# Kernel tuning notes

Measured on AMD Instinct MI355X. Metric: run time of the kernel, lower is better.

## Reference

```python
import jax, jax.numpy as jnp
import numpy as np

B, T, C, L = 256, 512, 256, 64
NEG = -1e30  # log-space 'zero'
BLANK = 0


def setup_inputs() -> dict:
    key = jax.random.key(0)
    k1, k2, k3, k4 = jax.random.split(key, 4)
    logits = jax.random.normal(k1, (B, T, C), dtype=jnp.float32)
    targets = jax.random.randint(k2, (B, L), 1, C)            # labels never equal blank (0)
    input_lengths = jax.random.randint(k3, (B,), T - 100, T + 1)
    target_lengths = jax.random.randint(k4, (B,), L // 2, L + 1)
    return dict(logits=logits, targets=targets,
                input_lengths=input_lengths, target_lengths=target_lengths)


def _ctc_loss(logits, targets, input_lengths, target_lengths):
    Bb, Tt, Cc = logits.shape
    Ll = targets.shape[1]
    S = 2 * Ll + 1  # extended label length (blanks interleaved)

    # fused log_softmax over vocab (original does permute then log_softmax; same math)
    logp = jax.nn.log_softmax(logits, axis=-1)  # [B,T,C]

    # extended target sequence: blank, y1, blank, y2, ..., blank
    ext = jnp.zeros((Bb, S), jnp.int32).at[:, 1::2].set(targets.astype(jnp.int32))
    # gather log-probs of extended labels for every timestep: [B,T,S]
    lp_ext = jnp.take_along_axis(logp, jnp.broadcast_to(ext[:, None, :], (Bb, Tt, S)), axis=2)

    # skip transition s-2 -> s allowed iff ext[s] != blank and ext[s] != ext[s-2]
    skip = jnp.zeros((Bb, S), bool).at[:, 2:].set(
        (ext[:, 2:] != BLANK) & (ext[:, 2:] != ext[:, :-2]))

    # alpha at t=0
    alpha0 = (jnp.full((Bb, S), NEG, dtype=logits.dtype)
              .at[:, 0].set(lp_ext[:, 0, 0])
              .at[:, 1].set(lp_ext[:, 0, 1]))

    neg1 = jnp.full((Bb, 1), NEG, dtype=logits.dtype)
    neg2 = jnp.full((Bb, 2), NEG, dtype=logits.dtype)

    def step(alpha, inputs):
        lp_t, t = inputs  # lp_t: [B,S]
        a1 = alpha
        a2 = jnp.concatenate([neg1, alpha[:, :-1]], axis=1)
        a3 = jnp.where(skip, jnp.concatenate([neg2, alpha[:, :-2]], axis=1), NEG)
        new = jnp.logaddexp(jnp.logaddexp(a1, a2), a3) + lp_t
        new = jnp.maximum(new, NEG)  # keep impossible paths bounded
        # freeze alpha for batch rows whose input sequence already ended
        alpha = jnp.where((t < input_lengths)[:, None], new, alpha)
        return alpha, None

    ts = jnp.arange(1, Tt)
    alphaT, _ = jax.lax.scan(step, alpha0, (jnp.swapaxes(lp_ext, 0, 1)[1:], ts))

    tl = target_lengths.astype(jnp.int32)
    a_last = jnp.take_along_axis(alphaT, (2 * tl)[:, None], axis=1)[:, 0]
    a_prev = jnp.take_along_axis(alphaT, (2 * tl - 1)[:, None], axis=1)[:, 0]
    loss = -jnp.logaddexp(a_last, a_prev)            # [B]
    loss = jnp.where(loss > 1e20, 0.0, loss)          # zero_infinity=True
    # reduction='mean': per-sample loss divided by target length, then batch mean
    return (loss / tl.astype(loss.dtype)).mean()


def reference(logits, targets, input_lengths, target_lengths):
    return _ctc_loss(logits, targets, input_lengths, target_lengths)
```

## Files before the change

### kernel.cpp

```cpp
#include <hip/hip_runtime.h>

#define B_ 256
#define T_ 512
#define C_ 256
#define L_ 64
#define S_ 129
#define TCH 64
#define LOG2E 1.44269504f
#define LN2 0.69314718f

template <int CTRL>
__device__ __forceinline__ int dpp_mov_i32(int x) {
    return __builtin_amdgcn_update_dpp(0, x, CTRL, 0xF, 0xF, true);
}

__device__ __forceinline__ double shr1d(double x) {
    int2 u = __builtin_bit_cast(int2, x);
    u.x = dpp_mov_i32<0x138>(u.x);
    u.y = dpp_mov_i32<0x138>(u.y);
    return __builtin_bit_cast(double, u);
}

template <int CTRL>
__device__ __forceinline__ double dpp_mov_f64(double x) {
    int2 u = __builtin_bit_cast(int2, x);
    u.x = dpp_mov_i32<CTRL>(u.x);
    u.y = dpp_mov_i32<CTRL>(u.y);
    return __builtin_bit_cast(double, u);
}

__device__ __forceinline__ float wave_sum(float x) {
#define DPPADD(ctrl)                                                          \
    x += __builtin_bit_cast(float, dpp_mov_i32<ctrl>(__builtin_bit_cast(int, x)));
    DPPADD(0x111) DPPADD(0x112) DPPADD(0x114)
    DPPADD(0x118) DPPADD(0x142) DPPADD(0x143)
#undef DPPADD
    return __builtin_bit_cast(float,
        __builtin_amdgcn_readlane(__builtin_bit_cast(int, x), 63));
}

__device__ __forceinline__ double wave_max_d(double x) {
    x = fmax(x, dpp_mov_f64<0x111>(x));
    x = fmax(x, dpp_mov_f64<0x112>(x));
    x = fmax(x, dpp_mov_f64<0x114>(x));
    x = fmax(x, dpp_mov_f64<0x118>(x));
    x = fmax(x, dpp_mov_f64<0x142>(x));
    x = fmax(x, dpp_mov_f64<0x143>(x));
    int2 u = __builtin_bit_cast(int2, x);
    u.x = __builtin_amdgcn_readlane(u.x, 63);
    u.y = __builtin_amdgcn_readlane(u.y, 63);
    return __builtin_bit_cast(double, u);
}

__device__ __forceinline__ void rescale(double& a0, double& a1, double& a2, int& e) {
    const double m = wave_max_d(fmax(fmax(a0, a1), a2));
    const int hi = __builtin_bit_cast(int2, m).y;
    int ex = ((hi >> 20) & 0x7ff) - 1023;
    if (m == 0.0) ex = 0;
    e += ex;
    int2 fb; fb.x = 0; fb.y = (1023 - ex) << 20;
    const double f = __builtin_bit_cast(double, fb);
    a0 *= f; a1 *= f; a2 *= f;
}

__device__ __forceinline__ float log2_pos(double a) {
    if (a == 0.0) return -1e30f;
    int2 u = __builtin_bit_cast(int2, a);
    const int ex = ((u.y >> 20) & 0x7ff) - 1023;
    u.y = (u.y & 0x800FFFFF) | (1023 << 20);
    const float mf = (float)__builtin_bit_cast(double, u);
    return __log2f(mf) + (float)ex;
}

__global__ __launch_bounds__(576) void k_fused(const float* __restrict__ logits,
                                               const int* __restrict__ targets,
                                               const int* __restrict__ in_len,
                                               const int* __restrict__ tg_len,
                                               float* __restrict__ out) {
    const int b = blockIdx.x;
    const int w = threadIdx.x >> 6;
    const int l = threadIdx.x & 63;

    __shared__ float Pb[2][TCH][64];
    __shared__ float Po[2][TCH][64];
    __shared__ int   tgt_sh[L_];
    __shared__ float alpha_sh[S_];

    if (threadIdx.x < L_) tgt_sh[threadIdx.x] = targets[(b << 6) + threadIdx.x];
    __syncthreads();

    const int len = in_len[b];
    double a0 = 0.0, a1 = 0.0, a2 = 0.0;
    int scale_total = 0;
    bool skip = false;
    if (w == 0) {
        const int tc = tgt_sh[l];
        const int tp = __shfl_up(tc, 1);
        skip = (l >= 1) && (tc != tp);
        __builtin_amdgcn_s_setprio(1);
    }
    const int mytgt = tgt_sh[l];

    const size_t rowbase = (size_t)b * T_;

    for (int k = 0; k < 9; ++k) {
        if (w > 0 && k < 8) {
            const int tt0 = (w - 1) * 8;
            float4 v[8];
            float  lv[8];
            #pragma unroll
            for (int r = 0; r < 8; ++r) {
                const int t = k * TCH + tt0 + r;
                v[r]  = ((const float4*)logits)[(rowbase + t) * 64 + l];
                lv[r] = logits[(rowbase + t) * C_ + mytgt];
            }
            #pragma unroll
            for (int r = 0; r < 8; ++r) {
                const int tt = tt0 + r;
                const float e0 = exp2f(v[r].x * LOG2E);
                const float e1 = exp2f(v[r].y * LOG2E);
                const float e2 = exp2f(v[r].z * LOG2E);
                const float e3 = exp2f(v[r].w * LOG2E);
                const float stot = wave_sum(e0 + e1 + e2 + e3);
                const float rs = __builtin_amdgcn_rcpf(stot);
                const float eb = __builtin_bit_cast(float,
                    __builtin_amdgcn_readfirstlane(__builtin_bit_cast(int, e0)));
                Pb[k & 1][tt][l] = eb * rs;
                Po[k & 1][tt][l] = exp2f(lv[r] * LOG2E) * rs;
            }
        }
        if (w == 0 && k >= 1) {
            const int kb = (k - 1) & 1;
            const int base = (k - 1) * TCH;
            float pba[8], poa[8], pbb[8], pob[8];
            #pragma unroll
            for (int j = 0; j < 8; ++j) { pba[j] = Pb[kb][j][l]; poa[j] = Po[kb][j][l]; }
            if (base == 0) {
                a0 = (l == 0) ? (double)pba[0] : 0.0;
                a1 = (l == 0) ? (double)poa[0] : 0.0;
                a2 = 0.0;
            }
            for (int g = 0; g < 8; ++g) {
                if (g < 7) {
                    #pragma unroll
                    for (int j = 0; j < 8; ++j) {
                        pbb[j] = Pb[kb][(g + 1) * 8 + j][l];
                        pob[j] = Po[kb][(g + 1) * 8 + j][l];
                    }
                }
                #pragma unroll
                for (int j = 0; j < 8; ++j) {
                    const int t = base + g * 8 + j;
                    if (t >= 1 && t < len) {
                        const double p = shr1d(a1);
                        const double c = skip ? p : 0.0;
                        const double a0n = (a0 + p) * (double)pba[j];
                        const double a1n = ((a1 + a0) + c) * (double)poa[j];
                        const double a2n = (a2 + a1) * (double)pba[j];
                        a0 = a0n; a1 = a1n; a2 = a2n;
                    }
                }
                if (g == 3 || g == 7) rescale(a0, a1, a2, scale_total);
                if (g < 7) {
                    #pragma unroll
                    for (int j = 0; j < 8; ++j) { pba[j] = pbb[j]; poa[j] = pob[j]; }
                }
            }
        }
        __syncthreads();
    }

    if (w == 0) {
        alpha_sh[2 * l]     = log2_pos(a0);
        alpha_sh[2 * l + 1] = log2_pos(a1);
        if (l == 63) alpha_sh[128] = log2_pos(a2);
    }
    __syncthreads();
    if (threadIdx.x == 0) {
        const int tl = tg_len[b];
        const float al = alpha_sh[2 * tl];
        const float ap = alpha_sh[2 * tl - 1];
        const float m  = fmaxf(al, ap);
        const float lse2 = m + __log2f(exp2f(al - m) + exp2f(ap - m));
        float loss = -LN2 * (lse2 + (float)scale_total);
        if (!(loss < 1e20f)) loss = 0.0f;
        atomicAdd(out, loss / (float)tl * (1.0f / (float)B_));
    }
}

extern "C" void kernel_launch(void* const* d_in, const int* in_sizes, int n_in,
                              void* d_out, int out_size, void* d_ws, size_t ws_size,
                              hipStream_t stream) {
    const float* logits  = (const float*)d_in[0];
    const int*   targets = (const int*)d_in[1];
    const int*   in_len  = (const int*)d_in[2];
    const int*   tg_len  = (const int*)d_in[3];
    float*       out     = (float*)d_out;

    (void)hipMemsetAsync(d_out, 0, sizeof(float), stream);
    k_fused<<<B_, 576, 0, stream>>>(logits, targets, in_len, tg_len, out);
}
```

Measured before the change: 204.2 us.

## Prefetch next logits chunk, gather target probs via LDS, pack P as float2

The producer waves now prefetch the next chunk's logits rows into registers while computing the current chunk. The separate scattered global load of the target-label logit is replaced by reading the already-computed exponentials from a small LDS staging buffer. The blank and label probabilities are packed into one float2 LDS array, so the recurrence wave issues fewer LDS loads. The cost is more registers per producer thread, extra LDS writes and reads per timestep, and a possible race on the reused rb4 slots, since a wave may read another lane's freshly written values without a barrier.

```diff
diff --git a/kernel.cpp b/kernel.cpp
--- a/kernel.cpp
+++ b/kernel.cpp
@@ -81,8 +81,8 @@
     const int w = threadIdx.x >> 6;
     const int l = threadIdx.x & 63;
 
-    __shared__ float Pb[2][TCH][64];
-    __shared__ float Po[2][TCH][64];
+    __shared__ float2 P[2][TCH][64];
+    __shared__ float4 rb4[8][2][64];
     __shared__ int   tgt_sh[L_];
     __shared__ float alpha_sh[S_];
 
@@ -103,50 +103,60 @@
 
     const size_t rowbase = (size_t)b * T_;
 
+    float4 va[8];
+    if (w > 0) {
+        const int tt0 = (w - 1) * 8;
+        #pragma unroll
+        for (int r = 0; r < 8; ++r)
+            va[r] = ((const float4*)logits)[(rowbase + tt0 + r) * 64 + l];
+    }
+
     for (int k = 0; k < 9; ++k) {
         if (w > 0 && k < 8) {
             const int tt0 = (w - 1) * 8;
-            float4 v[8];
-            float  lv[8];
-            #pragma unroll
-            for (int r = 0; r < 8; ++r) {
-                const int t = k * TCH + tt0 + r;
-                v[r]  = ((const float4*)logits)[(rowbase + t) * 64 + l];
-                lv[r] = logits[(rowbase + t) * C_ + mytgt];
+            float4 vb[8];
+            if (k < 7) {
+                #pragma unroll
+                for (int r = 0; r < 8; ++r) {
+                    const int t = (k + 1) * TCH + tt0 + r;
+                    vb[r] = ((const float4*)logits)[(rowbase + t) * 64 + l];
+                }
             }
             #pragma unroll
             for (int r = 0; r < 8; ++r) {
                 const int tt = tt0 + r;
-                const float e0 = exp2f(v[r].x * LOG2E);
-                const float e1 = exp2f(v[r].y * LOG2E);
-                const float e2 = exp2f(v[r].z * LOG2E);
-                const float e3 = exp2f(v[r].w * LOG2E);
-                const float stot = wave_sum(e0 + e1 + e2 + e3);
+                float4 e;
+                e.x = exp2f(va[r].x * LOG2E);
+                e.y = exp2f(va[r].y * LOG2E);
+                e.z = exp2f(va[r].z * LOG2E);
+                e.w = exp2f(va[r].w * LOG2E);
+                rb4[w - 1][r & 1][l] = e;
+                const float stot = wave_sum(e.x + e.y + e.z + e.w);
                 const float rs = __builtin_amdgcn_rcpf(stot);
                 const float eb = __builtin_bit_cast(float,
-                    __builtin_amdgcn_readfirstlane(__builtin_bit_cast(int, e0)));
-                Pb[k & 1][tt][l] = eb * rs;
-                Po[k & 1][tt][l] = exp2f(lv[r] * LOG2E) * rs;
-            }
+                    __builtin_amdgcn_readfirstlane(__builtin_bit_cast(int, e.x)));
+                const float eo = ((const float*)&rb4[w - 1][r & 1][0])[mytgt];
+                float2 pq; pq.x = eb * rs; pq.y = eo * rs;
+                P[k & 1][tt][l] = pq;
+            }
+            #pragma unroll
+            for (int r = 0; r < 8; ++r) va[r] = vb[r];
         }
         if (w == 0 && k >= 1) {
             const int kb = (k - 1) & 1;
             const int base = (k - 1) * TCH;
-            float pba[8], poa[8], pbb[8], pob[8];
+            float2 pa[8], pn[8];
             #pragma unroll
-            for (int j = 0; j < 8; ++j) { pba[j] = Pb[kb][j][l]; poa[j] = Po[kb][j][l]; }
+            for (int j = 0; j < 8; ++j) pa[j] = P[kb][j][l];
             if (base == 0) {
-                a0 = (l == 0) ? (double)pba[0] : 0.0;
-                a1 = (l == 0) ? (double)poa[0] : 0.0;
+                a0 = (l == 0) ? (double)pa[0].x : 0.0;
+                a1 = (l == 0) ? (double)pa[0].y : 0.0;
                 a2 = 0.0;
             }
             for (int g = 0; g < 8; ++g) {
                 if (g < 7) {
                     #pragma unroll
-                    for (int j = 0; j < 8; ++j) {
-                        pbb[j] = Pb[kb][(g + 1) * 8 + j][l];
-                        pob[j] = Po[kb][(g + 1) * 8 + j][l];
-                    }
+                    for (int j = 0; j < 8; ++j) pn[j] = P[kb][(g + 1) * 8 + j][l];
                 }
                 #pragma unroll
                 for (int j = 0; j < 8; ++j) {
@@ -154,16 +164,16 @@
                     if (t >= 1 && t < len) {
                         const double p = shr1d(a1);
                         const double c = skip ? p : 0.0;
-                        const double a0n = (a0 + p) * (double)pba[j];
-                        const double a1n = ((a1 + a0) + c) * (double)poa[j];
-                        const double a2n = (a2 + a1) * (double)pba[j];
+                        const double a0n = (a0 + p) * (double)pa[j].x;
+                        const double a1n = ((a1 + a0) + c) * (double)pa[j].y;
+                        const double a2n = (a2 + a1) * (double)pa[j].x;
                         a0 = a0n; a1 = a1n; a2 = a2n;
                     }
                 }
                 if (g == 3 || g == 7) rescale(a0, a1, a2, scale_total);
                 if (g < 7) {
                     #pragma unroll
-                    for (int j = 0; j < 8; ++j) { pba[j] = pbb[j]; poa[j] = pob[j]; }
+                    for (int j = 0; j < 8; ++j) pa[j] = pn[j];
                 }
             }
         }
```

New measurement: 203.5 us. About the same (-0.3%).

## Split fused CTC kernel into softmax-gather pass and fp16-fed alpha recursion

Applied to the files above, without the earlier changes.

Replaces the single producer/consumer kernel with two launches. The first is a fully parallel softmax kernel that writes scaled blank and label probabilities as packed fp16 into workspace. The second is a single-wave-per-batch alpha recursion that register-prefetches 32 timesteps ahead from global memory and rescales once per chunk. The aim is to remove the in-block synchronisation, shared-memory staging and serialisation of softmax behind the recurrence. In exchange it adds a global round trip, fp16 precision loss mitigated by a power-of-two prescale that is corrected in the loss, and a dependence on the workspace buffer.

```diff
diff --git a/kernel.cpp b/kernel.cpp
--- a/kernel.cpp
+++ b/kernel.cpp
@@ -5,9 +5,19 @@
 #define C_ 256
 #define L_ 64
 #define S_ 129
-#define TCH 64
+#define CH 32
 #define LOG2E 1.44269504f
 #define LN2 0.69314718f
+#define PSCALE 64.0f
+#define PSH 6
+
+__device__ __forceinline__ unsigned short f2h(float f) {
+    _Float16 h = (_Float16)f;
+    return __builtin_bit_cast(unsigned short, h);
+}
+__device__ __forceinline__ float h2f(unsigned short u) {
+    return (float)__builtin_bit_cast(_Float16, u);
+}
 
 template <int CTRL>
 __device__ __forceinline__ int dpp_mov_i32(int x) {
@@ -72,117 +82,100 @@
     return __log2f(mf) + (float)ex;
 }
 
-__global__ __launch_bounds__(576) void k_fused(const float* __restrict__ logits,
-                                               const int* __restrict__ targets,
-                                               const int* __restrict__ in_len,
-                                               const int* __restrict__ tg_len,
-                                               float* __restrict__ out) {
+__global__ __launch_bounds__(256) void k_soft(const float* __restrict__ logits,
+                                              const int* __restrict__ targets,
+                                              ushort2* __restrict__ G) {
+    const int wave = threadIdx.x >> 6;
+    const int lane = threadIdx.x & 63;
+    const int row  = (blockIdx.x << 2) + wave;
+    const int b    = row >> 9;
+
+    __shared__ float sh[4][C_];
+
+    const float4 v = ((const float4*)logits)[row * 64 + lane];
+    float4 e;
+    e.x = exp2f(v.x * LOG2E);
+    e.y = exp2f(v.y * LOG2E);
+    e.z = exp2f(v.z * LOG2E);
+    e.w = exp2f(v.w * LOG2E);
+    ((float4*)sh[wave])[lane] = e;
+
+    const float s  = wave_sum(e.x + e.y + e.z + e.w);
+    const float rs = PSCALE * __builtin_amdgcn_rcpf(s);
+    const float eb = __builtin_bit_cast(float,
+        __builtin_amdgcn_readfirstlane(__builtin_bit_cast(int, e.x)));
+    const int   tgt = targets[(b << 6) + lane];
+    const float eo  = sh[wave][tgt];
+
+    ushort2 pk;
+    pk.x = f2h(eb * rs);
+    pk.y = f2h(eo * rs);
+    G[row * 64 + lane] = pk;
+}
+
+__global__ __launch_bounds__(64) void k_alpha(const ushort2* __restrict__ G,
+                                              const int* __restrict__ targets,
+                                              const int* __restrict__ in_len,
+                                              const int* __restrict__ tg_len,
+                                              float* __restrict__ out) {
     const int b = blockIdx.x;
-    const int w = threadIdx.x >> 6;
-    const int l = threadIdx.x & 63;
+    const int l = threadIdx.x;
+    const ushort2* g = G + (size_t)b * T_ * 64;
+    const int len = in_len[b];
+    const int tl  = tg_len[b];
 
-    __shared__ float Pb[2][TCH][64];
-    __shared__ float Po[2][TCH][64];
-    __shared__ int   tgt_sh[L_];
-    __shared__ float alpha_sh[S_];
+    const int  tc   = targets[(b << 6) + l];
+    const int  tp   = __shfl_up(tc, 1);
+    const bool skip = (l >= 1) && (tc != tp);
 
-    if (threadIdx.x < L_) tgt_sh[threadIdx.x] = targets[(b << 6) + threadIdx.x];
-    __syncthreads();
-
-    const int len = in_len[b];
     double a0 = 0.0, a1 = 0.0, a2 = 0.0;
     int scale_total = 0;
-    bool skip = false;
-    if (w == 0) {
-        const int tc = tgt_sh[l];
-        const int tp = __shfl_up(tc, 1);
-        skip = (l >= 1) && (tc != tp);
-        __builtin_amdgcn_s_setprio(1);
-    }
-    const int mytgt = tgt_sh[l];
 
-    const size_t rowbase = (size_t)b * T_;
+    ushort2 bufA[CH], bufB[CH];
+    #pragma unroll
+    for (int j = 0; j < CH; ++j) bufA[j] = g[j * 64 + l];
 
-    for (int k = 0; k < 9; ++k) {
-        if (w > 0 && k < 8) {
-            const int tt0 = (w - 1) * 8;
-            float4 v[8];
-            float  lv[8];
-            #pragma unroll
-            for (int r = 0; r < 8; ++r) {
-                const int t = k * TCH + tt0 + r;
-                v[r]  = ((const float4*)logits)[(rowbase + t) * 64 + l];
-                lv[r] = logits[(rowbase + t) * C_ + mytgt];
-            }
-            #pragma unroll
-            for (int r = 0; r < 8; ++r) {
-                const int tt = tt0 + r;
-                const float e0 = exp2f(v[r].x * LOG2E);
-                const float e1 = exp2f(v[r].y * LOG2E);
-                const float e2 = exp2f(v[r].z * LOG2E);
-                const float e3 = exp2f(v[r].w * LOG2E);
-                const float stot = wave_sum(e0 + e1 + e2 + e3);
-                const float rs = __builtin_amdgcn_rcpf(stot);
-                const float eb = __builtin_bit_cast(float,
-                    __builtin_amdgcn_readfirstlane(__builtin_bit_cast(int, e0)));
-                Pb[k & 1][tt][l] = eb * rs;
-                Po[k & 1][tt][l] = exp2f(lv[r] * LOG2E) * rs;
+    for (int base = 0; base < len; base += CH) {
+        #pragma unroll
+        for (int j = 0; j < CH; ++j) {
+            int t = base + CH + j; t = t < T_ ? t : T_ - 1;
+            bufB[j] = g[t * 64 + l];
+        }
+        if (base == 0) {
+            a0 = (l == 0) ? (double)h2f(bufA[0].x) : 0.0;
+            a1 = (l == 0) ? (double)h2f(bufA[0].y) : 0.0;
+            a2 = 0.0;
+        }
+        #pragma unroll
+        for (int j = 0; j < CH; ++j) {
+            const int t = base + j;
+            if (t >= 1 && t < len) {
+                const double pb = (double)h2f(bufA[j].x);
+                const double po = (double)h2f(bufA[j].y);
+                const double p  = shr1d(a1);
+                const double c  = skip ? p : 0.0;
+                const double a0n = (a0 + p) * pb;
+                const double a1n = ((a1 + a0) + c) * po;
+                const double a2n = (a2 + a1) * pb;
+                a0 = a0n; a1 = a1n; a2 = a2n;
             }
         }
-        if (w == 0 && k >= 1) {
-            const int kb = (k - 1) & 1;
-            const int base = (k - 1) * TCH;
-            float pba[8], poa[8], pbb[8], pob[8];
-            #pragma unroll
-            for (int j = 0; j < 8; ++j) { pba[j] = Pb[kb][j][l]; poa[j] = Po[kb][j][l]; }
-            if (base == 0) {
-                a0 = (l == 0) ? (double)pba[0] : 0.0;
-                a1 = (l == 0) ? (double)poa[0] : 0.0;
-                a2 = 0.0;
-            }
-            for (int g = 0; g < 8; ++g) {
-                if (g < 7) {
-                    #pragma unroll
-                    for (int j = 0; j < 8; ++j) {
-                        pbb[j] = Pb[kb][(g + 1) * 8 + j][l];
-                        pob[j] = Po[kb][(g + 1) * 8 + j][l];
-                    }
-                }
-                #pragma unroll
-                for (int j = 0; j < 8; ++j) {
-                    const int t = base + g * 8 + j;
-                    if (t >= 1 && t < len) {
-                        const double p = shr1d(a1);
-                        const double c = skip ? p : 0.0;
-                        const double a0n = (a0 + p) * (double)pba[j];
-                        const double a1n = ((a1 + a0) + c) * (double)poa[j];
-                        const double a2n = (a2 + a1) * (double)pba[j];
-                        a0 = a0n; a1 = a1n; a2 = a2n;
-                    }
-                }
-                if (g == 3 || g == 7) rescale(a0, a1, a2, scale_total);
-                if (g < 7) {
-                    #pragma unroll
-                    for (int j = 0; j < 8; ++j) { pba[j] = pbb[j]; poa[j] = pob[j]; }
-                }
-            }
-        }
-        __syncthreads();
+        rescale(a0, a1, a2, scale_total);
+        #pragma unroll
+        for (int j = 0; j < CH; ++j) bufA[j] = bufB[j];
     }
 
-    if (w == 0) {
-        alpha_sh[2 * l]     = log2_pos(a0);
-        alpha_sh[2 * l + 1] = log2_pos(a1);
-        if (l == 63) alpha_sh[128] = log2_pos(a2);
-    }
+    __shared__ float alpha_sh[S_];
+    alpha_sh[2 * l]     = log2_pos(a0);
+    alpha_sh[2 * l + 1] = log2_pos(a1);
+    if (l == 63) alpha_sh[128] = log2_pos(a2);
     __syncthreads();
-    if (threadIdx.x == 0) {
-        const int tl = tg_len[b];
+    if (l == 0) {
         const float al = alpha_sh[2 * tl];
         const float ap = alpha_sh[2 * tl - 1];
         const float m  = fmaxf(al, ap);
         const float lse2 = m + __log2f(exp2f(al - m) + exp2f(ap - m));
-        float loss = -LN2 * (lse2 + (float)scale_total);
+        float loss = -LN2 * (lse2 + (float)scale_total - (float)(PSH * len));
         if (!(loss < 1e20f)) loss = 0.0f;
         atomicAdd(out, loss / (float)tl * (1.0f / (float)B_));
     }
@@ -196,7 +189,9 @@
     const int*   in_len  = (const int*)d_in[2];
     const int*   tg_len  = (const int*)d_in[3];
     float*       out     = (float*)d_out;
+    ushort2*     G       = (ushort2*)d_ws;
 
     (void)hipMemsetAsync(d_out, 0, sizeof(float), stream);
-    k_fused<<<B_, 576, 0, stream>>>(logits, targets, in_len, tg_len, out);
+    k_soft<<<(B_ * T_) / 4, 256, 0, stream>>>(logits, targets, G);
+    k_alpha<<<B_, 64, 0, stream>>>(G, targets, in_len, tg_len, out);
 }
```

New measurement: 218.2 us. 6.8% more time.
